# Performance work log

Hardware: AMD Instinct MI355X
Metric: run time of the kernel (lower is better)

Reference implementation:

```python
import jax, jax.numpy as jnp
import numpy as np

L = 30  # SSA window size (module default)


def _ssa_groups1(xm):
    """pyts-style SSA with groups=1: full-SVD reconstruction of the
    trajectory (Hankel) matrix followed by anti-diagonal averaging.
    xm: [B, N] -> [B, N]
    """
    B, N = xm.shape
    K = N - L + 1
    # Hankel trajectory matrix: X[b, i, j] = xm[b, i + j], shape [B, L, K]
    idx = jnp.arange(L)[:, None] + jnp.arange(K)[None, :]
    X = xm[:, idx]
    # SVD and rank-L reconstruction (groups=1 sums ALL elementary matrices)
    U, s, Vt = jnp.linalg.svd(X, full_matrices=False)  # U:[B,L,L] s:[B,L] Vt:[B,L,K]
    Xr = jnp.einsum('blr,br,brk->blk', U, s, Vt)       # [B, L, K]
    # Anti-diagonal (Hankel) averaging: average Xr[i, j] over i + j = t
    seg = idx.reshape(-1)                               # [L*K] values in [0, N)
    sums = jax.vmap(lambda m: jax.ops.segment_sum(m.reshape(-1), seg, num_segments=N))(Xr)
    counts = jax.ops.segment_sum(jnp.ones(L * K, dtype=xm.dtype), seg, num_segments=N)
    return sums / counts                                # [B, N]


def setup_inputs() -> dict:
    key = jax.random.key(0)
    x = jax.random.normal(key, (256, 64, 2048), dtype=jnp.float32)
    return {"x": x}


def reference(x):
    # x: [B, C, N]
    xm = jnp.max(x, axis=1)                 # channel-max, [B, N]
    x_ss = _ssa_groups1(xm)                 # SSA round-trip, [B, N]
    # Original code detaches the SSA branch (CPU/numpy round trip)
    x_ss = jax.lax.stop_gradient(x_ss)
    gate = jax.nn.softmax(x_ss, axis=-1)[:, None, :]  # [B, 1, N]
    return gate * x                         # [B, C, N]
```

## Files before the change

### kernel.cpp

```cpp
#include <hip/hip_runtime.h>
#include <math.h>


#define B_DIM 256
#define C_DIM 64
#define N_DIM 2048
#define COLS4 (N_DIM / 4)
#define THREADS 1024

__global__ __launch_bounds__(THREADS)
void ssa_gate_kernel(const float* __restrict__ x, float* __restrict__ out) {
    const int b    = blockIdx.x;
    const int t    = threadIdx.x;
    const int col  = t & (COLS4 - 1);
    const int grp  = t >> 9;
    const int lane = t & 63;
    const int wid  = t >> 6;

    const size_t base = (size_t)b * (C_DIM * N_DIM);
    const float4* __restrict__ xb = (const float4*)(x + base);
    float4* __restrict__ ob = (float4*)(out + base);

    __shared__ float4 pm[2][COLS4];
    __shared__ float  sred[16];

    const int c0 = grp * 32;

    float4 m;
    m.x = -INFINITY; m.y = -INFINITY; m.z = -INFINITY; m.w = -INFINITY;
    #pragma unroll 8
    for (int c = 0; c < 32; ++c) {
        const int cc = c0 + ((c + b) & 31);
        float4 v = xb[(size_t)cc * COLS4 + col];
        m.x = fmaxf(m.x, v.x);
        m.y = fmaxf(m.y, v.y);
        m.z = fmaxf(m.z, v.z);
        m.w = fmaxf(m.w, v.w);
    }
    pm[grp][col] = m;
    __syncthreads();

    float4 e;
    if (t < COLS4) {
        float4 a = pm[0][t];
        float4 c2 = pm[1][t];
        e.x = fmaxf(a.x, c2.x);
        e.y = fmaxf(a.y, c2.y);
        e.z = fmaxf(a.z, c2.z);
        e.w = fmaxf(a.w, c2.w);
        float tm = fmaxf(fmaxf(e.x, e.y), fmaxf(e.z, e.w));
        #pragma unroll
        for (int off = 32; off > 0; off >>= 1)
            tm = fmaxf(tm, __shfl_down(tm, off, 64));
        if (lane == 0) sred[wid] = tm;
    }
    __syncthreads();
    float M = sred[0];
    #pragma unroll
    for (int i = 1; i < 8; ++i) M = fmaxf(M, sred[i]);

    if (t < COLS4) {
        e.x = __expf(e.x - M);
        e.y = __expf(e.y - M);
        e.z = __expf(e.z - M);
        e.w = __expf(e.w - M);
        float ts = (e.x + e.y) + (e.z + e.w);
        #pragma unroll
        for (int off = 32; off > 0; off >>= 1)
            ts += __shfl_down(ts, off, 64);
        if (lane == 0) sred[8 + wid] = ts;
    }
    __syncthreads();
    float S = 0.0f;
    #pragma unroll
    for (int i = 8; i < 16; ++i) S += sred[i];

    if (t < COLS4) {
        const float inv = 1.0f / S;
        float4 gg;
        gg.x = e.x * inv; gg.y = e.y * inv; gg.z = e.z * inv; gg.w = e.w * inv;
        pm[0][t] = gg;
    }
    __syncthreads();

    const float4 g = pm[0][col];

    #pragma unroll 8
    for (int c = 0; c < 32; ++c) {
        const int cc = c0 + ((c + b) & 31);
        const size_t idx = (size_t)cc * COLS4 + col;
        float4 v = xb[idx];
        float4 o;
        o.x = v.x * g.x;
        o.y = v.y * g.y;
        o.z = v.z * g.z;
        o.w = v.w * g.w;
        ob[idx] = o;
    }
}

extern "C" void kernel_launch(void* const* d_in, const int* in_sizes, int n_in,
                              void* d_out, int out_size, void* d_ws, size_t ws_size,
                              hipStream_t stream) {
    const float* x = (const float*)d_in[0];
    float* out = (float*)d_out;
    ssa_gate_kernel<<<B_DIM, THREADS, 0, stream>>>(x, out);
}
```

Baseline: 245.7 us.

## Split fused gate kernel into max, softmax and multiply kernels using workspace

```diff
diff --git a/kernel.cpp b/kernel.cpp
--- a/kernel.cpp
+++ b/kernel.cpp
@@ -6,8 +6,88 @@
 #define C_DIM 64
 #define N_DIM 2048
 #define COLS4 (N_DIM / 4)
+#define ROW4  (C_DIM * COLS4)
+
+__global__ __launch_bounds__(256)
+void max_kernel(const float* __restrict__ x, float4* __restrict__ xm) {
+    const int row = blockIdx.x >> 1;
+    const int col = ((blockIdx.x & 1) << 8) + threadIdx.x;
+    const float4* __restrict__ xb = (const float4*)x + (size_t)row * ROW4 + col;
+    float4 m = make_float4(-INFINITY, -INFINITY, -INFINITY, -INFINITY);
+    #pragma unroll 8
+    for (int c = 0; c < C_DIM; ++c) {
+        float4 v = xb[(size_t)c * COLS4];
+        m.x = fmaxf(m.x, v.x); m.y = fmaxf(m.y, v.y);
+        m.z = fmaxf(m.z, v.z); m.w = fmaxf(m.w, v.w);
+    }
+    xm[(size_t)row * COLS4 + col] = m;
+}
+
+__global__ __launch_bounds__(256)
+void softmax_kernel(const float4* __restrict__ xm, float4* __restrict__ gate) {
+    const int b    = blockIdx.x;
+    const int t    = threadIdx.x;
+    const int lane = t & 63;
+    const int wid  = t >> 6;
+    __shared__ float sred[8];
+
+    const float4* __restrict__ rowp = xm + (size_t)b * COLS4;
+    float4 a0 = rowp[t];
+    float4 a1 = rowp[t + 256];
+
+    float tm = fmaxf(fmaxf(fmaxf(a0.x, a0.y), fmaxf(a0.z, a0.w)),
+                     fmaxf(fmaxf(a1.x, a1.y), fmaxf(a1.z, a1.w)));
+    #pragma unroll
+    for (int off = 32; off > 0; off >>= 1)
+        tm = fmaxf(tm, __shfl_down(tm, off, 64));
+    if (lane == 0) sred[wid] = tm;
+    __syncthreads();
+    const float M = fmaxf(fmaxf(sred[0], sred[1]), fmaxf(sred[2], sred[3]));
+
+    float4 e0, e1;
+    e0.x = __expf(a0.x - M); e0.y = __expf(a0.y - M);
+    e0.z = __expf(a0.z - M); e0.w = __expf(a0.w - M);
+    e1.x = __expf(a1.x - M); e1.y = __expf(a1.y - M);
+    e1.z = __expf(a1.z - M); e1.w = __expf(a1.w - M);
+    float ts = ((e0.x + e0.y) + (e0.z + e0.w)) + ((e1.x + e1.y) + (e1.z + e1.w));
+    #pragma unroll
+    for (int off = 32; off > 0; off >>= 1)
+        ts += __shfl_down(ts, off, 64);
+    if (lane == 0) sred[4 + wid] = ts;
+    __syncthreads();
+    const float inv = 1.0f / ((sred[4] + sred[5]) + (sred[6] + sred[7]));
+
+    float4 g0, g1;
+    g0.x = e0.x * inv; g0.y = e0.y * inv; g0.z = e0.z * inv; g0.w = e0.w * inv;
+    g1.x = e1.x * inv; g1.y = e1.y * inv; g1.z = e1.z * inv; g1.w = e1.w * inv;
+    gate[(size_t)b * COLS4 + t]       = g0;
+    gate[(size_t)b * COLS4 + t + 256] = g1;
+}
+
+#define MUL_BLOCKS  2048
+#define MUL_THREADS 256
+#define TOTAL4      (B_DIM * ROW4)
+#define MUL_STRIDE  ((size_t)MUL_BLOCKS * MUL_THREADS)
+#define MUL_ITERS   (TOTAL4 / (MUL_BLOCKS * MUL_THREADS))
+
+__global__ __launch_bounds__(MUL_THREADS)
+void mul_kernel(const float* __restrict__ x, const float4* __restrict__ gate,
+                float4* __restrict__ out4) {
+    size_t i = (size_t)blockIdx.x * MUL_THREADS + threadIdx.x;
+    const float4* __restrict__ x4 = (const float4*)x;
+    #pragma unroll 4
+    for (int it = 0; it < MUL_ITERS; ++it, i += MUL_STRIDE) {
+        const int b   = (int)(i >> 15);
+        const int col = (int)(i & (COLS4 - 1));
+        float4 g = gate[((size_t)b << 9) + col];
+        float4 v = x4[i];
+        float4 o;
+        o.x = v.x * g.x; o.y = v.y * g.y; o.z = v.z * g.z; o.w = v.w * g.w;
+        out4[i] = o;
+    }
+}
+
 #define THREADS 1024
-
 __global__ __launch_bounds__(THREADS)
 void ssa_gate_kernel(const float* __restrict__ x, float* __restrict__ out) {
     const int b    = blockIdx.x;
@@ -19,23 +99,20 @@
 
     const size_t base = (size_t)b * (C_DIM * N_DIM);
     const float4* __restrict__ xb = (const float4*)(x + base);
-    float4* __restrict__ ob = (float4*)(out + base);
+    float4* ob = (float4*)(out + base);
 
     __shared__ float4 pm[2][COLS4];
     __shared__ float  sred[16];
 
     const int c0 = grp * 32;
-
     float4 m;
     m.x = -INFINITY; m.y = -INFINITY; m.z = -INFINITY; m.w = -INFINITY;
     #pragma unroll 8
     for (int c = 0; c < 32; ++c) {
         const int cc = c0 + ((c + b) & 31);
         float4 v = xb[(size_t)cc * COLS4 + col];
-        m.x = fmaxf(m.x, v.x);
-        m.y = fmaxf(m.y, v.y);
-        m.z = fmaxf(m.z, v.z);
-        m.w = fmaxf(m.w, v.w);
+        m.x = fmaxf(m.x, v.x); m.y = fmaxf(m.y, v.y);
+        m.z = fmaxf(m.z, v.z); m.w = fmaxf(m.w, v.w);
     }
     pm[grp][col] = m;
     __syncthreads();
@@ -44,10 +121,8 @@
     if (t < COLS4) {
         float4 a = pm[0][t];
         float4 c2 = pm[1][t];
-        e.x = fmaxf(a.x, c2.x);
-        e.y = fmaxf(a.y, c2.y);
-        e.z = fmaxf(a.z, c2.z);
-        e.w = fmaxf(a.w, c2.w);
+        e.x = fmaxf(a.x, c2.x); e.y = fmaxf(a.y, c2.y);
+        e.z = fmaxf(a.z, c2.z); e.w = fmaxf(a.w, c2.w);
         float tm = fmaxf(fmaxf(e.x, e.y), fmaxf(e.z, e.w));
         #pragma unroll
         for (int off = 32; off > 0; off >>= 1)
@@ -60,10 +135,8 @@
     for (int i = 1; i < 8; ++i) M = fmaxf(M, sred[i]);
 
     if (t < COLS4) {
-        e.x = __expf(e.x - M);
-        e.y = __expf(e.y - M);
-        e.z = __expf(e.z - M);
-        e.w = __expf(e.w - M);
+        e.x = __expf(e.x - M); e.y = __expf(e.y - M);
+        e.z = __expf(e.z - M); e.w = __expf(e.w - M);
         float ts = (e.x + e.y) + (e.z + e.w);
         #pragma unroll
         for (int off = 32; off > 0; off >>= 1)
@@ -84,17 +157,13 @@
     __syncthreads();
 
     const float4 g = pm[0][col];
-
     #pragma unroll 8
     for (int c = 0; c < 32; ++c) {
         const int cc = c0 + ((c + b) & 31);
         const size_t idx = (size_t)cc * COLS4 + col;
         float4 v = xb[idx];
         float4 o;
-        o.x = v.x * g.x;
-        o.y = v.y * g.y;
-        o.z = v.z * g.z;
-        o.w = v.w * g.w;
+        o.x = v.x * g.x; o.y = v.y * g.y; o.z = v.z * g.z; o.w = v.w * g.w;
         ob[idx] = o;
     }
 }
@@ -104,5 +173,20 @@
                               hipStream_t stream) {
     const float* x = (const float*)d_in[0];
     float* out = (float*)d_out;
-    ssa_gate_kernel<<<B_DIM, THREADS, 0, stream>>>(x, out);
+    const size_t buf_bytes = (size_t)B_DIM * COLS4 * sizeof(float4);
+    if (ws_size >= 2 * buf_bytes) {
+        float4* xm   = (float4*)d_ws;
+        float4* gate = (float4*)((char*)d_ws + buf_bytes);
+        max_kernel<<<B_DIM * 2, 256, 0, stream>>>(x, xm);
+        softmax_kernel<<<B_DIM, 256, 0, stream>>>(xm, gate);
+        mul_kernel<<<MUL_BLOCKS, MUL_THREADS, 0, stream>>>(x, gate, (float4*)out);
+    } else if (ws_size >= buf_bytes) {
+        float4* gate = (float4*)d_ws;
+        float4* xm   = (float4*)out;
+        max_kernel<<<B_DIM * 2, 256, 0, stream>>>(x, xm);
+        softmax_kernel<<<B_DIM, 256, 0, stream>>>(xm, gate);
+        mul_kernel<<<MUL_BLOCKS, MUL_THREADS, 0, stream>>>(x, gate, (float4*)out);
+    } else {
+        ssa_gate_kernel<<<B_DIM, THREADS, 0, stream>>>(x, out);
+    }
 }
```

New measurement: 257.3 us. 4.7% more time.

## Split gate computation and gating multiply into two kernels for more parallelism

Applied to the files above, without the earlier changes.

```diff
diff --git a/kernel.cpp b/kernel.cpp
--- a/kernel.cpp
+++ b/kernel.cpp
@@ -6,10 +6,10 @@
 #define C_DIM 64
 #define N_DIM 2048
 #define COLS4 (N_DIM / 4)
-#define THREADS 1024
+#define ROW4  (C_DIM * COLS4)
 
-__global__ __launch_bounds__(THREADS)
-void ssa_gate_kernel(const float* __restrict__ x, float* __restrict__ out) {
+__global__ __launch_bounds__(1024)
+void gate_kernel(const float* __restrict__ x, float* __restrict__ out) {
     const int b    = blockIdx.x;
     const int t    = threadIdx.x;
     const int col  = t & (COLS4 - 1);
@@ -17,37 +17,29 @@
     const int lane = t & 63;
     const int wid  = t >> 6;
 
-    const size_t base = (size_t)b * (C_DIM * N_DIM);
-    const float4* __restrict__ xb = (const float4*)(x + base);
-    float4* __restrict__ ob = (float4*)(out + base);
+    const float4* __restrict__ xb = (const float4*)x + (size_t)b * ROW4;
+    float4* ob = (float4*)out + (size_t)b * ROW4;
 
     __shared__ float4 pm[2][COLS4];
     __shared__ float  sred[16];
 
     const int c0 = grp * 32;
-
-    float4 m;
-    m.x = -INFINITY; m.y = -INFINITY; m.z = -INFINITY; m.w = -INFINITY;
+    float4 m = make_float4(-INFINITY, -INFINITY, -INFINITY, -INFINITY);
     #pragma unroll 8
     for (int c = 0; c < 32; ++c) {
-        const int cc = c0 + ((c + b) & 31);
-        float4 v = xb[(size_t)cc * COLS4 + col];
-        m.x = fmaxf(m.x, v.x);
-        m.y = fmaxf(m.y, v.y);
-        m.z = fmaxf(m.z, v.z);
-        m.w = fmaxf(m.w, v.w);
+        float4 v = xb[(size_t)(c0 + c) * COLS4 + col];
+        m.x = fmaxf(m.x, v.x); m.y = fmaxf(m.y, v.y);
+        m.z = fmaxf(m.z, v.z); m.w = fmaxf(m.w, v.w);
     }
     pm[grp][col] = m;
     __syncthreads();
 
     float4 e;
     if (t < COLS4) {
-        float4 a = pm[0][t];
+        float4 a  = pm[0][t];
         float4 c2 = pm[1][t];
-        e.x = fmaxf(a.x, c2.x);
-        e.y = fmaxf(a.y, c2.y);
-        e.z = fmaxf(a.z, c2.z);
-        e.w = fmaxf(a.w, c2.w);
+        e.x = fmaxf(a.x, c2.x); e.y = fmaxf(a.y, c2.y);
+        e.z = fmaxf(a.z, c2.z); e.w = fmaxf(a.w, c2.w);
         float tm = fmaxf(fmaxf(e.x, e.y), fmaxf(e.z, e.w));
         #pragma unroll
         for (int off = 32; off > 0; off >>= 1)
@@ -60,10 +52,8 @@
     for (int i = 1; i < 8; ++i) M = fmaxf(M, sred[i]);
 
     if (t < COLS4) {
-        e.x = __expf(e.x - M);
-        e.y = __expf(e.y - M);
-        e.z = __expf(e.z - M);
-        e.w = __expf(e.w - M);
+        e.x = __expf(e.x - M); e.y = __expf(e.y - M);
+        e.z = __expf(e.z - M); e.w = __expf(e.w - M);
         float ts = (e.x + e.y) + (e.z + e.w);
         #pragma unroll
         for (int off = 32; off > 0; off >>= 1)
@@ -71,31 +61,44 @@
         if (lane == 0) sred[8 + wid] = ts;
     }
     __syncthreads();
-    float S = 0.0f;
-    #pragma unroll
-    for (int i = 8; i < 16; ++i) S += sred[i];
 
     if (t < COLS4) {
+        float S = 0.0f;
+        #pragma unroll
+        for (int i = 8; i < 16; ++i) S += sred[i];
         const float inv = 1.0f / S;
         float4 gg;
         gg.x = e.x * inv; gg.y = e.y * inv; gg.z = e.z * inv; gg.w = e.w * inv;
-        pm[0][t] = gg;
+        ob[(size_t)( 0) * COLS4 + t] = gg;
+        ob[(size_t)(16) * COLS4 + t] = gg;
+        ob[(size_t)(32) * COLS4 + t] = gg;
+        ob[(size_t)(48) * COLS4 + t] = gg;
     }
+}
+
+__global__ __launch_bounds__(512)
+void mul_kernel(const float* __restrict__ x, float* __restrict__ out) {
+    const int bid = blockIdx.x;
+    const int b   = bid >> 2;
+    const int g   = bid & 3;
+    const int col = threadIdx.x;
+
+    const size_t rbase = (size_t)b * ROW4;
+    const float4* __restrict__ x4 = (const float4*)x + rbase;
+    float4* o4 = (float4*)out + rbase;
+
+    const int cbase = g * 16;
+    const float4 gv = o4[(size_t)cbase * COLS4 + col];
     __syncthreads();
 
-    const float4 g = pm[0][col];
-
-    #pragma unroll 8
-    for (int c = 0; c < 32; ++c) {
-        const int cc = c0 + ((c + b) & 31);
-        const size_t idx = (size_t)cc * COLS4 + col;
-        float4 v = xb[idx];
+    #pragma unroll 4
+    for (int c = 0; c < 16; ++c) {
+        const size_t idx = (size_t)(cbase + c) * COLS4 + col;
+        float4 v = x4[idx];
         float4 o;
-        o.x = v.x * g.x;
-        o.y = v.y * g.y;
-        o.z = v.z * g.z;
-        o.w = v.w * g.w;
-        ob[idx] = o;
+        o.x = v.x * gv.x; o.y = v.y * gv.y;
+        o.z = v.z * gv.z; o.w = v.w * gv.w;
+        o4[idx] = o;
     }
 }
 
@@ -104,5 +107,6 @@
                               hipStream_t stream) {
     const float* x = (const float*)d_in[0];
     float* out = (float*)d_out;
-    ssa_gate_kernel<<<B_DIM, THREADS, 0, stream>>>(x, out);
+    gate_kernel<<<B_DIM, 1024, 0, stream>>>(x, out);
+    mul_kernel<<<B_DIM * 4, 512, 0, stream>>>(x, out);
 }
```

Result: no change. 250.2 us (+1.8%).
